# Kernel tuning notes

Hardware: AMD Instinct MI355X
Metric: run time of the kernel (lower is better)

The kernel has to match this reference:

```python
import jax, jax.numpy as jnp
import numpy as np

B, T, D, H = 4, 2048, 1024, 16
DK = D // H

def setup_inputs() -> dict:
    key = jax.random.key(0)
    ks = jax.random.split(key, 5)
    s = 1.0 / np.sqrt(D)
    return {
        "x": jax.random.normal(ks[0], (B, T, D), jnp.float32),
        "Wq": jax.random.normal(ks[1], (D, D), jnp.float32) * s,
        "Wk": jax.random.normal(ks[2], (D, D), jnp.float32) * s,
        "Wv": jax.random.normal(ks[3], (D, D), jnp.float32) * s,
        "Wo": jax.random.normal(ks[4], (D, D), jnp.float32) * s,
    }

def reference(x, Wq, Wk, Wv, Wo):
    # torch Linear: y = x @ W.T (W is [out, in], no bias)
    q = jnp.einsum('btd,ed->bte', x, Wq).reshape(B, T, H, DK).transpose(0, 2, 1, 3)
    k = jnp.einsum('btd,ed->bte', x, Wk).reshape(B, T, H, DK).transpose(0, 2, 1, 3)
    v = jnp.einsum('btd,ed->bte', x, Wv).reshape(B, T, H, DK).transpose(0, 2, 1, 3)
    # scores: [B, H, T, T]
    scores = jnp.einsum('bhqd,bhkd->bhqk', q, k) * (DK ** -0.5)
    causal_mask = jnp.triu(jnp.ones((T, T), dtype=bool), k=1)  # True above diagonal
    scores = jnp.where(causal_mask, -jnp.inf, scores)
    attn = jax.nn.softmax(scores, axis=-1)  # dropout = identity (p=0 / eval)
    ctx = jnp.einsum('bhqk,bhkd->bhqd', attn, v)  # [B, H, T, DK]
    ctx = ctx.transpose(0, 2, 1, 3).reshape(B, T, D)
    out = jnp.einsum('btd,ed->bte', ctx, Wo)
    return out
```

## Files before the change

### kernel.cpp

```cpp
#include <hip/hip_runtime.h>
#include <hip/hip_bf16.h>
#include <stdint.h>

#define BB 4
#define TT 2048
#define DD 1024
#define HH 16
#define DKK 64

typedef unsigned short u16;
typedef unsigned int u32;
typedef __bf16 bf16_t;
typedef bf16_t bf16x8 __attribute__((ext_vector_type(8)));
typedef float f32x4 __attribute__((ext_vector_type(4)));

#if __has_builtin(__builtin_amdgcn_exp2f)
#define EXPW(x) __builtin_amdgcn_exp2f(x)
#define QSCL 0.1803368801111244f
#else
#define EXPW(x) __expf(x)
#define QSCL 0.125f
#endif

__device__ __forceinline__ float bf2f(u16 u) {
    u32 x = ((u32)u) << 16;
    float f;
    __builtin_memcpy(&f, &x, 4);
    return f;
}
__device__ __forceinline__ u16 f2bf(float f) {
    u32 x;
    __builtin_memcpy(&x, &f, 4);
    x += 0x7fffu + ((x >> 16) & 1u);
    return (u16)(x >> 16);
}

__device__ __forceinline__ void gll16(const u16* g, u16* l) {
    __builtin_amdgcn_global_load_lds((const __attribute__((address_space(1))) u32*)g,
                                     (__attribute__((address_space(3))) u32*)l, 16, 0, 0);
}

__global__ void cast_f32_bf16(const float* __restrict__ in, u16* __restrict__ out, int n) {
    int i = (blockIdx.x * blockDim.x + threadIdx.x) * 4;
    int stride = gridDim.x * blockDim.x * 4;
    for (; i < n; i += stride) {
        float4 v = *reinterpret_cast<const float4*>(in + i);
        uint2 pk;
        pk.x = (u32)f2bf(v.x) | ((u32)f2bf(v.y) << 16);
        pk.y = (u32)f2bf(v.z) | ((u32)f2bf(v.w) << 16);
        *reinterpret_cast<uint2*>(out + i) = pk;
    }
}

__global__ void cast_w4(const float* __restrict__ w0, const float* __restrict__ w1,
                        const float* __restrict__ w2, const float* __restrict__ w3,
                        u16* __restrict__ out, int nW) {
    const float* src = (blockIdx.y == 0) ? w0 : (blockIdx.y == 1) ? w1 : (blockIdx.y == 2) ? w2 : w3;
    u16* dst = out + (size_t)blockIdx.y * nW;
    int i = (blockIdx.x * blockDim.x + threadIdx.x) * 4;
    int stride = gridDim.x * blockDim.x * 4;
    for (; i < nW; i += stride) {
        float4 v = *reinterpret_cast<const float4*>(src + i);
        uint2 pk;
        pk.x = (u32)f2bf(v.x) | ((u32)f2bf(v.y) << 16);
        pk.y = (u32)f2bf(v.z) | ((u32)f2bf(v.w) << 16);
        *reinterpret_cast<uint2*>(dst + i) = pk;
    }
}

__device__ __forceinline__ void gemm_128_mainloop(const u16* __restrict__ A,
                                                  const u16* __restrict__ W,
                                                  u16* As, u16* Bs,
                                                  int m0, int n0, f32x4 acc[4][4]) {
    const int tid = threadIdx.x;
    const int lane = tid & 63;
    const int wid = tid >> 6;
    const int wr = (wid >> 1) * 64, wc = (wid & 1) * 64;
    const int l15 = lane & 15, l4 = lane >> 4;

    const f32x4 z4 = {0.f, 0.f, 0.f, 0.f};
#pragma unroll
    for (int i = 0; i < 4; i++)
#pragma unroll
        for (int j = 0; j < 4; j++) acc[i][j] = z4;

    const int r0 = tid >> 2;
    const int c0 = (tid & 3) * 8;

    for (int k0 = 0; k0 < DD; k0 += 32) {
        __syncthreads();
        gll16(A + (m0 + r0) * DD + k0 + c0, As + (wid * 64) * 8);
        gll16(A + (m0 + 64 + r0) * DD + k0 + c0, As + (256 + wid * 64) * 8);
        gll16(W + (n0 + r0) * DD + k0 + c0, Bs + (wid * 64) * 8);
        gll16(W + (n0 + 64 + r0) * DD + k0 + c0, Bs + (256 + wid * 64) * 8);
        asm volatile("s_waitcnt vmcnt(0)" ::: "memory");
        __syncthreads();

        bf16x8 af[4], bfr[4];
#pragma unroll
        for (int mi = 0; mi < 4; mi++)
            af[mi] = *reinterpret_cast<const bf16x8*>(As + (wr + mi * 16 + l15) * 32 + l4 * 8);
#pragma unroll
        for (int ni = 0; ni < 4; ni++)
            bfr[ni] = *reinterpret_cast<const bf16x8*>(Bs + (wc + ni * 16 + l15) * 32 + l4 * 8);
#pragma unroll
        for (int mi = 0; mi < 4; mi++)
#pragma unroll
            for (int ni = 0; ni < 4; ni++)
                acc[mi][ni] =
                    __builtin_amdgcn_mfma_f32_16x16x32_bf16(af[mi], bfr[ni], acc[mi][ni], 0, 0, 0);
    }
}

__global__ __launch_bounds__(256) void gemm_qkv(const u16* __restrict__ xb,
                                                const u16* __restrict__ wq,
                                                const u16* __restrict__ wk,
                                                const u16* __restrict__ wv,
                                                u16* __restrict__ Qo, u16* __restrict__ Ko,
                                                u16* __restrict__ Vto) {
    __shared__ u16 As[128 * 32];
    __shared__ u16 Bs[128 * 32];
    const int z = blockIdx.z;
    const u16* W = (z == 0) ? wq : (z == 1) ? wk : wv;
    u16* dst = (z == 0) ? Qo : (z == 1) ? Ko : Vto;
    const int m0 = blockIdx.x * 128, n0 = blockIdx.y * 128;

    f32x4 acc[4][4];
    gemm_128_mainloop(xb, W, As, Bs, m0, n0, acc);

    const int lane = threadIdx.x & 63, wid = threadIdx.x >> 6;
    const int wr = (wid >> 1) * 64, wc = (wid & 1) * 64;
    const int l15 = lane & 15, l4 = lane >> 4;
#pragma unroll
    for (int mi = 0; mi < 4; mi++)
#pragma unroll
        for (int ni = 0; ni < 4; ni++)
#pragma unroll
            for (int j = 0; j < 4; j++) {
                int m = m0 + wr + mi * 16 + l4 * 4 + j;
                int n = n0 + wc + ni * 16 + l15;
                int b = m >> 11, t = m & (TT - 1);
                int h = n >> 6, dk = n & 63;
                u16 v = f2bf(acc[mi][ni][j]);
                if (z < 2)
                    dst[((b * HH + h) * TT + t) * DKK + dk] = v;
                else
                    dst[((b * HH + h) * DKK + dk) * TT + t] = v;
            }
}

__global__ __launch_bounds__(256) void gemm_out(const u16* __restrict__ ctx,
                                                const u16* __restrict__ wo,
                                                float* __restrict__ out) {
    __shared__ u16 As[128 * 32];
    __shared__ u16 Bs[128 * 32];
    const int m0 = blockIdx.x * 128, n0 = blockIdx.y * 128;
    f32x4 acc[4][4];
    gemm_128_mainloop(ctx, wo, As, Bs, m0, n0, acc);

    const int lane = threadIdx.x & 63, wid = threadIdx.x >> 6;
    const int wr = (wid >> 1) * 64, wc = (wid & 1) * 64;
    const int l15 = lane & 15, l4 = lane >> 4;
#pragma unroll
    for (int mi = 0; mi < 4; mi++)
#pragma unroll
        for (int ni = 0; ni < 4; ni++)
#pragma unroll
            for (int j = 0; j < 4; j++) {
                int m = m0 + wr + mi * 16 + l4 * 4 + j;
                int n = n0 + wc + ni * 16 + l15;
                out[m * DD + n] = acc[mi][ni][j];
            }
}


__device__ __forceinline__ void stage_kv(const u16* __restrict__ Kb, const u16* __restrict__ Vb,
                                         u16* Kd, u16* Vd, int kt, int tid, int wid) {
    int r = tid >> 3, cc = tid & 7;
    int cs = cc ^ (r & 7);
    gll16(Kb + (kt * 64 + r) * DKK + cs * 8, Kd + wid * 64 * 8);
    gll16(Vb + r * TT + kt * 64 + cs * 8, Vd + wid * 64 * 8);
}

__device__ __forceinline__ void load_qfrag16(const u16* Qb, int qbase, int l15, int l4,
                                             bf16x8 qf[2]) {
#pragma unroll
    for (int kc = 0; kc < 2; kc++) {
        const u16* p = Qb + (qbase + l15) * DKK + kc * 32 + l4 * 8;
        union { uint4 u; u16 h[8]; } cv;
        cv.u = *reinterpret_cast<const uint4*>(p);
        u16 o[8];
#pragma unroll
        for (int e = 0; e < 8; e++) o[e] = f2bf(bf2f(cv.h[e]) * QSCL);
        __builtin_memcpy(&qf[kc], o, 16);
    }
}

__device__ __forceinline__ void write_ctx16(u16* __restrict__ ctx, int b, int h, int qbase,
                                            int l15, int l4, const f32x4 acc[4],
                                            const f32x4 lacc) {
#pragma unroll
    for (int j = 0; j < 4; j++) {
        float inv = 1.0f / lacc[j];
        int t = qbase + l4 * 4 + j;
#pragma unroll
        for (int cf = 0; cf < 4; cf++) {
            int dk = cf * 16 + l15;
            ctx[((size_t)(b * TT + t)) * DD + h * 64 + dk] = f2bf(acc[cf][j] * inv);
        }
    }
}

__device__ __forceinline__ void attn_side(const bf16x8 qf[2], f32x4 acc[4], f32x4& lacc,
                                          const char* Kl, const char* Vl, char* Pw,
                                          bf16x8 onef, int l15, int l4,
                                          bool domask, int kt, int qbase) {
    const f32x4 z4 = {0.f, 0.f, 0.f, 0.f};
    f32x4 s[4];
#pragma unroll
    for (int cf = 0; cf < 4; cf++) s[cf] = z4;

#pragma unroll
    for (int kc = 0; kc < 2; kc++) {
#pragma unroll
        for (int cf = 0; cf < 4; cf++) {
            int kr = cf * 16 + l15;
            int cw = (l4 + kc * 4) ^ (kr & 7);
            bf16x8 kf = *reinterpret_cast<const bf16x8*>(Kl + kr * 128 + cw * 16);
            s[cf] = __builtin_amdgcn_mfma_f32_16x16x32_bf16(qf[kc], kf, s[cf], 0, 0, 0);
        }
    }

    asm volatile("s_waitcnt lgkmcnt(0)" ::: "memory");

#pragma unroll
    for (int cf = 0; cf < 4; cf++)
#pragma unroll
        for (int j = 0; j < 4; j++) {
            float v = s[cf][j];
            if (domask) {
                int kk = kt * 64 + cf * 16 + l15;
                int qq = qbase + l4 * 4 + j;
                if (kk > qq) v = -__builtin_huge_valf();
            }
            float p = EXPW(v);
            int r = l4 * 4 + j;
            int col = cf * 16 + l15;
            int byte = r * 128 + (((col >> 3) ^ (r & 7)) << 4) + (col & 7) * 2;
            *reinterpret_cast<u16*>(Pw + byte) = f2bf(p);
        }

    asm volatile("s_waitcnt lgkmcnt(0)" ::: "memory");
    __builtin_amdgcn_sched_barrier(0);

#pragma unroll
    for (int kc = 0; kc < 2; kc++) {
        int cwp = (l4 + kc * 4) ^ (l15 & 7);
        bf16x8 pa = *reinterpret_cast<const bf16x8*>(Pw + l15 * 128 + cwp * 16);
#pragma unroll
        for (int cf = 0; cf < 4; cf++) {
            int vr = cf * 16 + l15;
            int vw = (l4 + kc * 4) ^ (vr & 7);
            bf16x8 vf = *reinterpret_cast<const bf16x8*>(Vl + vr * 128 + vw * 16);
            acc[cf] = __builtin_amdgcn_mfma_f32_16x16x32_bf16(pa, vf, acc[cf], 0, 0, 0);
        }
        lacc = __builtin_amdgcn_mfma_f32_16x16x32_bf16(pa, onef, lacc, 0, 0, 0);
    }
}

__global__ __launch_bounds__(512, 2) void attn_fwd(const u16* __restrict__ Qg,
                                                   const u16* __restrict__ Kg,
                                                   const u16* __restrict__ Vtg,
                                                   u16* __restrict__ ctx) {
    __shared__ u16 Kld[4][64 * 64];
    __shared__ u16 Vld[4][64 * 64];
    __shared__ u16 Pld[8][16 * 64];

    const int tid = threadIdx.x;
    const int lane = tid & 63, wid = tid >> 6;
    const int l15 = lane & 15, l4 = lane >> 4;
    const int bh = blockIdx.x;
    const int jA = blockIdx.y, jB = 15 - jA;
    const int qbaseA = jA * 128 + wid * 16;
    const int qbaseB = jB * 128 + wid * 16;
    const int nA = 2 * jA + 1 + (wid >> 2);
    const int nB = 2 * jB + 1 + (wid >> 2);
    const int nkt = 2 * jB + 2;

    const u16* Qb = Qg + (size_t)bh * TT * DKK;
    const u16* Kb = Kg + (size_t)bh * TT * DKK;
    const u16* Vb = Vtg + (size_t)bh * DKK * TT;

    bf16x8 qfA[2], qfB[2];
    load_qfrag16(Qb, qbaseA, l15, l4, qfA);
    load_qfrag16(Qb, qbaseB, l15, l4, qfB);

    bf16x8 onef;
    {
        union { bf16x8 v; u16 h[8]; } o;
#pragma unroll
        for (int e = 0; e < 8; e++) o.h[e] = 0x3F80;
        onef = o.v;
    }

    f32x4 accA[4], accB[4], laccA, laccB;
    const f32x4 z4 = {0.f, 0.f, 0.f, 0.f};
#pragma unroll
    for (int j = 0; j < 4; j++) { accA[j] = z4; accB[j] = z4; }
    laccA = z4; laccB = z4;

    char* Pw = reinterpret_cast<char*>(&Pld[wid][0]);

    stage_kv(Kb, Vb, Kld[0], Vld[0], 0, tid, wid);
    stage_kv(Kb, Vb, Kld[1], Vld[1], 1, tid, wid);

    for (int kt = 0; kt < nkt; kt++) {
        if (kt + 2 < nkt) {
            stage_kv(Kb, Vb, Kld[(kt + 2) & 3], Vld[(kt + 2) & 3], kt + 2, tid, wid);
            asm volatile("s_waitcnt vmcnt(4)" ::: "memory");
        } else if (kt + 1 < nkt) {
            asm volatile("s_waitcnt vmcnt(2)" ::: "memory");
        } else {
            asm volatile("s_waitcnt vmcnt(0)" ::: "memory");
        }
        __syncthreads();

        const char* Kl = reinterpret_cast<const char*>(Kld[kt & 3]);
        const char* Vl = reinterpret_cast<const char*>(Vld[kt & 3]);

        if (kt < nA)
            attn_side(qfA, accA, laccA, Kl, Vl, Pw, onef, l15, l4, kt == nA - 1, kt, qbaseA);
        if (kt < nB)
            attn_side(qfB, accB, laccB, Kl, Vl, Pw, onef, l15, l4, kt == nB - 1, kt, qbaseB);
    }

    const int b = bh >> 4, h = bh & 15;
    write_ctx16(ctx, b, h, qbaseA, l15, l4, accA, laccA);
    write_ctx16(ctx, b, h, qbaseB, l15, l4, accB, laccB);
}

extern "C" void kernel_launch(void* const* d_in, const int* in_sizes, int n_in,
                              void* d_out, int out_size, void* d_ws, size_t ws_size,
                              hipStream_t stream) {
    const float* x = (const float*)d_in[0];
    const float* Wq = (const float*)d_in[1];
    const float* Wk = (const float*)d_in[2];
    const float* Wv = (const float*)d_in[3];
    const float* Wo = (const float*)d_in[4];

    const int nX = BB * TT * DD;
    const int nW = DD * DD;
    const int nQ = BB * HH * TT * DKK;

    u16* xb = (u16*)d_ws;
    u16* wqb = xb + nX;
    u16* wkb = wqb + nW;
    u16* wvb = wkb + nW;
    u16* wob = wvb + nW;
    u16* Qb = wob + nW;
    u16* Kb = Qb + nQ;
    u16* Vtb = Kb + nQ;
    u16* ctxb = Vtb + nQ;

    cast_f32_bf16<<<4096, 256, 0, stream>>>(x, xb, nX);
    cast_w4<<<dim3(1024, 4), 256, 0, stream>>>(Wq, Wk, Wv, Wo, wqb, nW);

    gemm_qkv<<<dim3((BB * TT) / 128, DD / 128, 3), 256, 0, stream>>>(xb, wqb, wkb, wvb, Qb, Kb, Vtb);

    attn_fwd<<<dim3(64, 8), 512, 0, stream>>>(Qb, Kb, Vtb, ctxb);

    gemm_out<<<dim3((BB * TT) / 128, DD / 128), 256, 0, stream>>>(ctxb, wob, (float*)d_out);
}
```

Baseline: 198.8 us.

## Triple-buffer GEMM shared-memory tiles to overlap global loads with MFMA

After: 212.3 us. 6.8% more time.

```diff
diff --git a/kernel.cpp b/kernel.cpp
--- a/kernel.cpp
+++ b/kernel.cpp
@@ -68,6 +68,15 @@
     }
 }
 
+__device__ __forceinline__ void gemm_stage(const u16* __restrict__ A, const u16* __restrict__ W,
+                                           u16* As, u16* Bs, int m0, int n0, int k0,
+                                           int r0, int c0, int wid) {
+    gll16(A + (m0 + r0) * DD + k0 + c0, As + (wid * 64) * 8);
+    gll16(A + (m0 + 64 + r0) * DD + k0 + c0, As + (256 + wid * 64) * 8);
+    gll16(W + (n0 + r0) * DD + k0 + c0, Bs + (wid * 64) * 8);
+    gll16(W + (n0 + 64 + r0) * DD + k0 + c0, Bs + (256 + wid * 64) * 8);
+}
+
 __device__ __forceinline__ void gemm_128_mainloop(const u16* __restrict__ A,
                                                   const u16* __restrict__ W,
                                                   u16* As, u16* Bs,
@@ -87,28 +96,36 @@
     const int r0 = tid >> 2;
     const int c0 = (tid & 3) * 8;
 
-    for (int k0 = 0; k0 < DD; k0 += 32) {
+    int cur = 0;
+    gemm_stage(A, W, As, Bs, m0, n0, 0, r0, c0, wid);
+
+    for (int kk = 0; kk < 32; kk++) {
+        int nxt = cur + 1; if (nxt == 3) nxt = 0;
+        if (kk + 1 < 32) {
+            gemm_stage(A, W, As + nxt * 4096, Bs + nxt * 4096, m0, n0, (kk + 1) * 32,
+                       r0, c0, wid);
+            asm volatile("s_waitcnt vmcnt(4)" ::: "memory");
+        } else {
+            asm volatile("s_waitcnt vmcnt(0)" ::: "memory");
+        }
         __syncthreads();
-        gll16(A + (m0 + r0) * DD + k0 + c0, As + (wid * 64) * 8);
-        gll16(A + (m0 + 64 + r0) * DD + k0 + c0, As + (256 + wid * 64) * 8);
-        gll16(W + (n0 + r0) * DD + k0 + c0, Bs + (wid * 64) * 8);
-        gll16(W + (n0 + 64 + r0) * DD + k0 + c0, Bs + (256 + wid * 64) * 8);
-        asm volatile("s_waitcnt vmcnt(0)" ::: "memory");
-        __syncthreads();
-
+
+        const u16* Asc = As + cur * 4096;
+        const u16* Bsc = Bs + cur * 4096;
         bf16x8 af[4], bfr[4];
 #pragma unroll
         for (int mi = 0; mi < 4; mi++)
-            af[mi] = *reinterpret_cast<const bf16x8*>(As + (wr + mi * 16 + l15) * 32 + l4 * 8);
+            af[mi] = *reinterpret_cast<const bf16x8*>(Asc + (wr + mi * 16 + l15) * 32 + l4 * 8);
 #pragma unroll
         for (int ni = 0; ni < 4; ni++)
-            bfr[ni] = *reinterpret_cast<const bf16x8*>(Bs + (wc + ni * 16 + l15) * 32 + l4 * 8);
+            bfr[ni] = *reinterpret_cast<const bf16x8*>(Bsc + (wc + ni * 16 + l15) * 32 + l4 * 8);
 #pragma unroll
         for (int mi = 0; mi < 4; mi++)
 #pragma unroll
             for (int ni = 0; ni < 4; ni++)
                 acc[mi][ni] =
                     __builtin_amdgcn_mfma_f32_16x16x32_bf16(af[mi], bfr[ni], acc[mi][ni], 0, 0, 0);
+        cur = nxt;
     }
 }
 
@@ -118,15 +135,15 @@
                                                 const u16* __restrict__ wv,
                                                 u16* __restrict__ Qo, u16* __restrict__ Ko,
                                                 u16* __restrict__ Vto) {
-    __shared__ u16 As[128 * 32];
-    __shared__ u16 Bs[128 * 32];
+    __shared__ u16 As[3][128 * 32];
+    __shared__ u16 Bs[3][128 * 32];
     const int z = blockIdx.z;
     const u16* W = (z == 0) ? wq : (z == 1) ? wk : wv;
     u16* dst = (z == 0) ? Qo : (z == 1) ? Ko : Vto;
     const int m0 = blockIdx.x * 128, n0 = blockIdx.y * 128;
 
     f32x4 acc[4][4];
-    gemm_128_mainloop(xb, W, As, Bs, m0, n0, acc);
+    gemm_128_mainloop(xb, W, &As[0][0], &Bs[0][0], m0, n0, acc);
 
     const int lane = threadIdx.x & 63, wid = threadIdx.x >> 6;
     const int wr = (wid >> 1) * 64, wc = (wid & 1) * 64;
@@ -152,11 +169,11 @@
 __global__ __launch_bounds__(256) void gemm_out(const u16* __restrict__ ctx,
                                                 const u16* __restrict__ wo,
                                                 float* __restrict__ out) {
-    __shared__ u16 As[128 * 32];
-    __shared__ u16 Bs[128 * 32];
+    __shared__ u16 As[3][128 * 32];
+    __shared__ u16 Bs[3][128 * 32];
     const int m0 = blockIdx.x * 128, n0 = blockIdx.y * 128;
     f32x4 acc[4][4];
-    gemm_128_mainloop(ctx, wo, As, Bs, m0, n0, acc);
+    gemm_128_mainloop(ctx, wo, &As[0][0], &Bs[0][0], m0, n0, acc);
 
     const int lane = threadIdx.x & 63, wid = threadIdx.x >> 6;
     const int wr = (wid >> 1) * 64, wc = (wid & 1) * 64;
```
